# Kernel tuning notes

Hardware: AMD Instinct MI355X
Metric: run time of the kernel (lower is better)

## Reference

```python
import jax, jax.numpy as jnp
import numpy as np

N_ITERATION = 3
NEG_INF = -1e18
EPS = 1e-8


def squash(t, eps=EPS):
    # t: [..., E]; scale = |t|^2/(1+|t|^2), out = scale * t / |t|
    sq = jnp.sum(t * t, axis=-1, keepdims=True)
    return (sq / (1.0 + sq)) * t / (jnp.sqrt(sq) + eps)


def setup_inputs() -> dict:
    key = jax.random.key(0)
    k1, k2, k3, k4 = jax.random.split(key, 4)
    B, K, L, D, O, E = 8, 1024, 1024, 1024, 6, 128
    inputs_u = jax.random.normal(k1, (B, K, D), dtype=jnp.float32)
    context_sequence = jax.random.normal(k2, (B, L, D), dtype=jnp.float32)
    # route_weights: [num_out_caps, d_model, d_per_capsule], fan-in scaled
    route_weights = jax.random.normal(k3, (O, D, E), dtype=jnp.float32) / np.sqrt(D)
    # True = padded in-capsule (masked)
    inputs_mask = jax.random.randint(k4, (B, K), 0, 2).astype(bool)
    return {
        "inputs_u": inputs_u,
        "context_sequence": context_sequence,
        "route_weights": route_weights,
        "inputs_mask": inputs_mask,
    }


def reference(inputs_u, context_sequence, route_weights, inputs_mask):
    # priors_u_hat: [B, K, O, E] (shared route weights across in-capsules)
    priors = jnp.einsum("bkd,ode->bkoe", inputs_u, route_weights)
    B, K, O, E = priors.shape
    L = context_sequence.shape[1]
    logits = jnp.zeros((B, L, K, O), dtype=priors.dtype)
    mask4 = inputs_mask[:, None, :, None]  # [B,1,K,1] -> broadcast to [B,L,K,O]
    outputs_v = None
    probs_c = None
    for i in range(N_ITERATION):
        lg = jnp.where(mask4, NEG_INF, logits)
        probs_c = jax.nn.softmax(lg, axis=-1)  # softmax over out-capsules
        # weighted aggregation over in-capsules then squash: [B,L,O,E]
        outputs_v = squash(jnp.einsum("blko,bkoe->bloe", probs_c, priors))
        if i != N_ITERATION - 1:
            # agreement delta logits: [B,L,K,O]
            logits = logits + jnp.einsum("bkoe,bloe->blko", priors, outputs_v)
    return outputs_v, probs_c
```

## Files before the change

kernel.cpp:

```cpp
#include <hip/hip_runtime.h>
#include <hip/hip_bf16.h>
#include <stdint.h>

typedef __bf16 bf16_t;
typedef __bf16 bf16x8 __attribute__((ext_vector_type(8)));
typedef float f32x4 __attribute__((ext_vector_type(4)));

#define BB 8
#define KK 1024
#define LL 1024
#define DD 1024
#define OO 6
#define EE 128
#define NN 768

__device__ __forceinline__ void async_copy16(const void* gptr, void* lds) {
    __builtin_amdgcn_global_load_lds(
        (__attribute__((address_space(1))) void*)gptr,
        (__attribute__((address_space(3))) void*)lds,
        16, 0, 0);
}

__device__ __forceinline__ void split_bf16(float x, bf16_t& hi, bf16_t& lo) {
    hi = (bf16_t)x;
    lo = (bf16_t)(x - (float)hi);
}

__global__ __launch_bounds__(256) void convert_a(
    const float* __restrict__ A, bf16_t* __restrict__ Ah, bf16_t* __restrict__ Al)
{
    const long i = ((long)blockIdx.x * 256 + threadIdx.x) * 4;
    const float4 x = *(const float4*)(A + i);
    union { bf16_t h[4]; uint2 u; } ph, pl;
    split_bf16(x.x, ph.h[0], pl.h[0]);
    split_bf16(x.y, ph.h[1], pl.h[1]);
    split_bf16(x.z, ph.h[2], pl.h[2]);
    split_bf16(x.w, ph.h[3], pl.h[3]);
    *(uint2*)(Ah + i) = ph.u;
    *(uint2*)(Al + i) = pl.u;
}

__global__ __launch_bounds__(256) void convert_w(
    const float* __restrict__ W, bf16_t* __restrict__ Wth, bf16_t* __restrict__ Wtl)
{
    __shared__ float t[32][33];
    const int o  = blockIdx.z;
    const int d0 = blockIdx.x * 32;
    const int e0 = blockIdx.y * 32;
    const int tx = threadIdx.x & 31;
    const int ty = threadIdx.x >> 5;
    const float* Wo = W + (long)o * DD * EE;
    bf16_t* Ho = Wth + (long)o * EE * DD;
    bf16_t* Lo = Wtl + (long)o * EE * DD;
#pragma unroll
    for (int p = 0; p < 4; ++p)
        t[p * 8 + ty][tx] = Wo[(long)(d0 + p * 8 + ty) * EE + e0 + tx];
    __syncthreads();
#pragma unroll
    for (int p = 0; p < 4; ++p) {
        const float val = t[tx][p * 8 + ty];
        bf16_t h, l;
        split_bf16(val, h, l);
        const long idx = (long)(e0 + p * 8 + ty) * DD + d0 + tx;
        Ho[idx] = h;
        Lo[idx] = l;
    }
}

__global__ __launch_bounds__(256) void gemm_priors(
    const bf16_t* __restrict__ Ah, const bf16_t* __restrict__ Al,
    const bf16_t* __restrict__ Bh, const bf16_t* __restrict__ Bl,
    float* __restrict__ C)
{
    __shared__ alignas(16) bf16_t sAh[128 * 32];
    __shared__ alignas(16) bf16_t sAl[128 * 32];
    __shared__ alignas(16) bf16_t sBh[64 * 32];
    __shared__ alignas(16) bf16_t sBl[64 * 32];

    const int tid  = threadIdx.x;
    const int w    = tid >> 6;
    const int lane = tid & 63;
    const int bm   = blockIdx.x;
    const int bn   = blockIdx.y;
    const int qr   = (w >> 1) * 64;
    const int qc   = (w & 1) * 32;
    const int r16  = lane & 15;
    const int q    = lane >> 4;

    f32x4 acc[4][2] = {};

    const int mrowA = w * 32 + (lane >> 2);
    const int mrowB = w * 16 + (lane >> 2);
    const int kcol  = (lane & 3) * 8;

    const long aoff = (long)(bm * 128 + mrowA) * DD + kcol;
    const long boff = (long)(bn * 64  + mrowB) * DD + kcol;
    const bf16_t* gAh0 = Ah + aoff;  const bf16_t* gAh1 = gAh0 + 16 * DD;
    const bf16_t* gAl0 = Al + aoff;  const bf16_t* gAl1 = gAl0 + 16 * DD;
    const bf16_t* gBh  = Bh + boff;
    const bf16_t* gBl  = Bl + boff;

    bf16_t* lAh0 = sAh + (w * 2 + 0) * 512;
    bf16_t* lAh1 = sAh + (w * 2 + 1) * 512;
    bf16_t* lAl0 = sAl + (w * 2 + 0) * 512;
    bf16_t* lAl1 = sAl + (w * 2 + 1) * 512;
    bf16_t* lBh  = sBh + w * 512;
    bf16_t* lBl  = sBl + w * 512;

    for (int kt = 0; kt < DD / 32; ++kt) {
        const int k0 = kt * 32;
        async_copy16(gAh0 + k0, lAh0);
        async_copy16(gAh1 + k0, lAh1);
        async_copy16(gAl0 + k0, lAl0);
        async_copy16(gAl1 + k0, lAl1);
        async_copy16(gBh  + k0, lBh);
        async_copy16(gBl  + k0, lBl);
        __syncthreads();

        bf16x8 ah[4], al[4], bh[2], bl[2];
#pragma unroll
        for (int i = 0; i < 4; ++i) {
            const int ra = (qr + 16 * i + r16) * 32 + q * 8;
            ah[i] = *(const bf16x8*)(sAh + ra);
            al[i] = *(const bf16x8*)(sAl + ra);
        }
#pragma unroll
        for (int j = 0; j < 2; ++j) {
            const int rb = (qc + 16 * j + r16) * 32 + q * 8;
            bh[j] = *(const bf16x8*)(sBh + rb);
            bl[j] = *(const bf16x8*)(sBl + rb);
        }
#pragma unroll
        for (int i = 0; i < 4; ++i)
#pragma unroll
            for (int j = 0; j < 2; ++j) {
                acc[i][j] = __builtin_amdgcn_mfma_f32_16x16x32_bf16(
                    al[i], bh[j], acc[i][j], 0, 0, 0);
                acc[i][j] = __builtin_amdgcn_mfma_f32_16x16x32_bf16(
                    ah[i], bl[j], acc[i][j], 0, 0, 0);
                acc[i][j] = __builtin_amdgcn_mfma_f32_16x16x32_bf16(
                    ah[i], bh[j], acc[i][j], 0, 0, 0);
            }
        __syncthreads();
    }

#pragma unroll
    for (int i = 0; i < 4; ++i)
#pragma unroll
        for (int j = 0; j < 2; ++j) {
            const int col = bn * 64 + qc + 16 * j + r16;
#pragma unroll
            for (int r = 0; r < 4; ++r) {
                const int row = bm * 128 + qr + 16 * i + q * 4 + r;
                C[(long)row * NN + col] = acc[i][j][r];
            }
        }
}

__global__ __launch_bounds__(256) void s_kernel(
    const float* __restrict__ priors, const float* __restrict__ probs,
    float* __restrict__ s_part, int uniform)
{
    const int bo = blockIdx.x;
    const int b = bo / OO, o = bo % OO;
    const int kbase = blockIdx.y * 128;
    const int t = threadIdx.x;
    const int e = t & 127;
    const int kh = t >> 7;
    float accv = 0.f;
    const int k0 = kbase + kh * 64;
    for (int kk = 0; kk < 64; ++kk) {
        const long row = (long)(b * KK + k0 + kk) * OO + o;
        const float wgt = uniform ? (1.0f / 6.0f) : probs[row];
        accv = fmaf(wgt, priors[row * EE + e], accv);
    }
    __shared__ float red[256];
    red[t] = accv;
    __syncthreads();
    if (t < 128)
        s_part[((long)blockIdx.y * 48 + bo) * EE + e] = red[t] + red[t + 128];
}

__global__ __launch_bounds__(128) void squash_kernel(
    const float* __restrict__ s_part, float* __restrict__ v)
{
    const int bo = blockIdx.x;
    const int e = threadIdx.x;
    float x = 0.f;
#pragma unroll
    for (int y = 0; y < 8; ++y) x += s_part[((long)y * 48 + bo) * EE + e];
    float sq = x * x;
#pragma unroll
    for (int off = 32; off > 0; off >>= 1) sq += __shfl_down(sq, off, 64);
    __shared__ float wsum[2];
    if ((threadIdx.x & 63) == 0) wsum[threadIdx.x >> 6] = sq;
    __syncthreads();
    const float total = wsum[0] + wsum[1];
    v[bo * EE + e] = total / (1.0f + total) * x / (sqrtf(total) + 1e-8f);
}

__global__ __launch_bounds__(256) void fused_pg_kernel(
    const float* __restrict__ priors, const float* __restrict__ v,
    const int* __restrict__ mask, float* __restrict__ g,
    float* __restrict__ probs, int read_g, int store_g)
{
    const int wid  = blockIdx.x * 4 + (threadIdx.x >> 6);
    const int lane = threadIdx.x & 63;
    const int b = wid >> 10;
    const float* pr = priors + (long)wid * NN;
    const float* vb = v + b * NN;

    float po[OO];
#pragma unroll
    for (int o = 0; o < OO; ++o) {
        const int j0 = o * EE + lane;
        po[o] = pr[j0] * vb[j0] + pr[j0 + 64] * vb[j0 + 64];
    }
#pragma unroll
    for (int off = 32; off > 0; off >>= 1)
#pragma unroll
        for (int o = 0; o < OO; ++o) po[o] += __shfl_xor(po[o], off, 64);

    if (read_g) {
#pragma unroll
        for (int o = 0; o < OO; ++o) po[o] += g[wid * OO + o];
    }
    if (store_g && lane < OO) g[wid * OO + lane] = po[lane];

    float p;
    if (mask[wid] != 0) {
        p = 1.0f / 6.0f;
    } else {
        float m = po[0];
#pragma unroll
        for (int o = 1; o < OO; ++o) m = fmaxf(m, po[o]);
        float ssum = 0.f;
#pragma unroll
        for (int o = 0; o < OO; ++o) { po[o] = expf(po[o] - m); ssum += po[o]; }
        const float inv = 1.0f / ssum;
        p = ((lane < OO) ? po[lane] : 0.f) * inv;
    }
    if (lane < OO) probs[wid * OO + lane] = p;
}

__global__ __launch_bounds__(256) void bcast_kernel(
    const float* __restrict__ V, const float* __restrict__ P,
    float* __restrict__ out)
{
    const long base = ((long)blockIdx.x * 256 + threadIdx.x) * 4;
    const long NV = (long)BB * LL * OO * EE;
    const float* src;
    if (base < NV) {
        const long b  = base / ((long)LL * OO * EE);
        const int off = (int)(base % NN);
        src = V + b * NN + off;
    } else {
        const long b2 = base - NV;
        const long b  = b2 / ((long)LL * KK * OO);
        const int off = (int)(b2 % (KK * OO));
        src = P + b * (KK * OO) + off;
    }
    *(float4*)(out + base) = *(const float4*)(src);
}

extern "C" void kernel_launch(void* const* d_in, const int* in_sizes, int n_in,
                              void* d_out, int out_size, void* d_ws, size_t ws_size,
                              hipStream_t stream)
{
    (void)in_sizes; (void)n_in; (void)out_size; (void)ws_size;
    const float* u    = (const float*)d_in[0];
    const float* W    = (const float*)d_in[2];
    const int*   mask = (const int*)d_in[3];
    float*       out  = (float*)d_out;

    char* ws = (char*)d_ws;
    size_t off = 0;
    float*  priors = (float*)(ws + off);  off += (size_t)8192 * NN * 4;
    bf16_t* Ah     = (bf16_t*)(ws + off); off += (size_t)8192 * DD * 2;
    bf16_t* Al     = (bf16_t*)(ws + off); off += (size_t)8192 * DD * 2;
    bf16_t* Wth    = (bf16_t*)(ws + off); off += (size_t)OO * EE * DD * 2;
    bf16_t* Wtl    = (bf16_t*)(ws + off); off += (size_t)OO * EE * DD * 2;
    float*  g      = (float*)(ws + off);  off += (size_t)BB * KK * OO * 4;
    float*  probs  = (float*)(ws + off);  off += (size_t)BB * KK * OO * 4;
    float*  s_part = (float*)(ws + off);  off += (size_t)8 * 48 * EE * 4;
    float*  v      = (float*)(ws + off);

    hipLaunchKernelGGL(convert_a, dim3(8192), dim3(256), 0, stream, u, Ah, Al);
    hipLaunchKernelGGL(convert_w, dim3(32, 4, 6), dim3(256), 0, stream, W, Wth, Wtl);
    hipLaunchKernelGGL(gemm_priors, dim3(64, 12), dim3(256), 0, stream,
                       Ah, Al, Wth, Wtl, priors);

    hipLaunchKernelGGL(s_kernel, dim3(48, 8), dim3(256), 0, stream,
                       priors, (const float*)nullptr, s_part, 1);
    hipLaunchKernelGGL(squash_kernel, dim3(48), dim3(128), 0, stream, s_part, v);

    hipLaunchKernelGGL(fused_pg_kernel, dim3(2048), dim3(256), 0, stream,
                       priors, v, mask, g, probs, 0, 1);
    hipLaunchKernelGGL(s_kernel, dim3(48, 8), dim3(256), 0, stream,
                       priors, probs, s_part, 0);
    hipLaunchKernelGGL(squash_kernel, dim3(48), dim3(128), 0, stream, s_part, v);

    hipLaunchKernelGGL(fused_pg_kernel, dim3(2048), dim3(256), 0, stream,
                       priors, v, mask, g, probs, 1, 0);
    hipLaunchKernelGGL(s_kernel, dim3(48, 8), dim3(256), 0, stream,
                       priors, probs, s_part, 0);
    hipLaunchKernelGGL(squash_kernel, dim3(48), dim3(128), 0, stream, s_part, v);

    hipLaunchKernelGGL(bcast_kernel, dim3(55296), dim3(256), 0, stream, v, probs, out);
}
```

Baseline: 372.7 us.

## Fuse routing iterations into GEMM epilogue and single-pass prob/aggregate kernels

Measured after the change: 376.2 us. No clear change (+1.0%).

```diff
diff --git a/kernel.cpp b/kernel.cpp
--- a/kernel.cpp
+++ b/kernel.cpp
@@ -24,6 +24,18 @@
 __device__ __forceinline__ void split_bf16(float x, bf16_t& hi, bf16_t& lo) {
     hi = (bf16_t)x;
     lo = (bf16_t)(x - (float)hi);
+}
+
+__device__ __forceinline__ void squash_regs(const float* sp, float* vv, int lane) {
+#pragma unroll
+    for (int o = 0; o < 6; ++o) {
+        float t = sp[2*o]*sp[2*o] + sp[2*o+1]*sp[2*o+1];
+#pragma unroll
+        for (int off = 32; off > 0; off >>= 1) t += __shfl_xor(t, off, 64);
+        const float sc = t / (1.0f + t) / (sqrtf(t) + 1e-8f);
+        vv[2*o]   = sc * sp[2*o];
+        vv[2*o+1] = sc * sp[2*o+1];
+    }
 }
 
 __global__ __launch_bounds__(256) void convert_a(
@@ -70,12 +82,13 @@
 __global__ __launch_bounds__(256) void gemm_priors(
     const bf16_t* __restrict__ Ah, const bf16_t* __restrict__ Al,
     const bf16_t* __restrict__ Bh, const bf16_t* __restrict__ Bl,
-    float* __restrict__ C)
+    float* __restrict__ C, float* __restrict__ s0)
 {
     __shared__ alignas(16) bf16_t sAh[128 * 32];
     __shared__ alignas(16) bf16_t sAl[128 * 32];
     __shared__ alignas(16) bf16_t sBh[64 * 32];
     __shared__ alignas(16) bf16_t sBl[64 * 32];
+    __shared__ float sRed[64];
 
     const int tid  = threadIdx.x;
     const int w    = tid >> 6;
@@ -155,112 +168,160 @@
                 C[(long)row * NN + col] = acc[i][j][r];
             }
         }
-}
-
-__global__ __launch_bounds__(256) void s_kernel(
-    const float* __restrict__ priors, const float* __restrict__ probs,
-    float* __restrict__ s_part, int uniform)
-{
-    const int bo = blockIdx.x;
-    const int b = bo / OO, o = bo % OO;
-    const int kbase = blockIdx.y * 128;
+
+    if (tid < 64) sRed[tid] = 0.f;
+    __syncthreads();
+#pragma unroll
+    for (int j = 0; j < 2; ++j) {
+        float cs = 0.f;
+#pragma unroll
+        for (int i = 0; i < 4; ++i)
+            cs += acc[i][j][0] + acc[i][j][1] + acc[i][j][2] + acc[i][j][3];
+        cs += __shfl_xor(cs, 16, 64);
+        cs += __shfl_xor(cs, 32, 64);
+        if (lane < 16)
+            atomicAdd(&sRed[qc + 16 * j + r16], cs);
+    }
+    __syncthreads();
+    if (tid < 64)
+        atomicAdd(&s0[(bm >> 3) * NN + bn * 64 + tid], sRed[tid] * (1.0f / 6.0f));
+}
+
+__global__ __launch_bounds__(256) void pgs_kernel(
+    const float* __restrict__ priors, const float* __restrict__ s_prev,
+    const int* __restrict__ mask, float* __restrict__ g,
+    float* __restrict__ probs, float* __restrict__ s_cur, int first)
+{
+    const int blk  = blockIdx.x;
+    const int b    = blk >> 7;
+    const int k8   = (blk & 127) * 8;
+    const int w    = threadIdx.x >> 6;
+    const int lane = threadIdx.x & 63;
+
+    float vv[12];
+    {
+        float sp[12];
+#pragma unroll
+        for (int s = 0; s < 12; ++s) sp[s] = s_prev[b * NN + s * 64 + lane];
+        squash_regs(sp, vv, lane);
+    }
+
+    float sacc[12];
+#pragma unroll
+    for (int s = 0; s < 12; ++s) sacc[s] = 0.f;
+
+#pragma unroll
+    for (int r = 0; r < 2; ++r) {
+        const int k = k8 + w * 2 + r;
+        const long rid = (long)b * KK + k;
+        const float* pr = priors + rid * NN;
+        float pp[12];
+#pragma unroll
+        for (int s = 0; s < 12; ++s) pp[s] = pr[s * 64 + lane];
+
+        float d[6];
+#pragma unroll
+        for (int o = 0; o < 6; ++o) {
+            float t = pp[2*o] * vv[2*o] + pp[2*o+1] * vv[2*o+1];
+#pragma unroll
+            for (int off = 32; off > 0; off >>= 1) t += __shfl_xor(t, off, 64);
+            d[o] = t;
+        }
+
+        if (first) {
+            if (lane < 6) {
+                float x = d[0];
+#pragma unroll
+                for (int o = 1; o < 6; ++o) if (lane == o) x = d[o];
+                g[rid * 6 + lane] = x;
+            }
+        } else {
+#pragma unroll
+            for (int o = 0; o < 6; ++o) d[o] += g[rid * 6 + o];
+        }
+
+        float p[6];
+        if (mask[rid] != 0) {
+#pragma unroll
+            for (int o = 0; o < 6; ++o) p[o] = 1.0f / 6.0f;
+        } else {
+            float m = d[0];
+#pragma unroll
+            for (int o = 1; o < 6; ++o) m = fmaxf(m, d[o]);
+            float ssum = 0.f;
+#pragma unroll
+            for (int o = 0; o < 6; ++o) { p[o] = expf(d[o] - m); ssum += p[o]; }
+            const float inv = 1.0f / ssum;
+#pragma unroll
+            for (int o = 0; o < 6; ++o) p[o] *= inv;
+        }
+
+        if (!first && lane < 6) {
+            float x = p[0];
+#pragma unroll
+            for (int o = 1; o < 6; ++o) if (lane == o) x = p[o];
+            probs[rid * 6 + lane] = x;
+        }
+
+#pragma unroll
+        for (int s = 0; s < 12; ++s) sacc[s] = fmaf(p[s >> 1], pp[s], sacc[s]);
+    }
+
+    __shared__ float red[4][768];
+#pragma unroll
+    for (int s = 0; s < 12; ++s) red[w][s * 64 + lane] = sacc[s];
+    __syncthreads();
     const int t = threadIdx.x;
-    const int e = t & 127;
-    const int kh = t >> 7;
-    float accv = 0.f;
-    const int k0 = kbase + kh * 64;
-    for (int kk = 0; kk < 64; ++kk) {
-        const long row = (long)(b * KK + k0 + kk) * OO + o;
-        const float wgt = uniform ? (1.0f / 6.0f) : probs[row];
-        accv = fmaf(wgt, priors[row * EE + e], accv);
-    }
-    __shared__ float red[256];
-    red[t] = accv;
-    __syncthreads();
-    if (t < 128)
-        s_part[((long)blockIdx.y * 48 + bo) * EE + e] = red[t] + red[t + 128];
-}
-
-__global__ __launch_bounds__(128) void squash_kernel(
-    const float* __restrict__ s_part, float* __restrict__ v)
-{
-    const int bo = blockIdx.x;
-    const int e = threadIdx.x;
-    float x = 0.f;
-#pragma unroll
-    for (int y = 0; y < 8; ++y) x += s_part[((long)y * 48 + bo) * EE + e];
-    float sq = x * x;
-#pragma unroll
-    for (int off = 32; off > 0; off >>= 1) sq += __shfl_down(sq, off, 64);
-    __shared__ float wsum[2];
-    if ((threadIdx.x & 63) == 0) wsum[threadIdx.x >> 6] = sq;
-    __syncthreads();
-    const float total = wsum[0] + wsum[1];
-    v[bo * EE + e] = total / (1.0f + total) * x / (sqrtf(total) + 1e-8f);
-}
-
-__global__ __launch_bounds__(256) void fused_pg_kernel(
-    const float* __restrict__ priors, const float* __restrict__ v,
-    const int* __restrict__ mask, float* __restrict__ g,
-    float* __restrict__ probs, int read_g, int store_g)
-{
-    const int wid  = blockIdx.x * 4 + (threadIdx.x >> 6);
-    const int lane = threadIdx.x & 63;
-    const int b = wid >> 10;
-    const float* pr = priors + (long)wid * NN;
-    const float* vb = v + b * NN;
-
-    float po[OO];
-#pragma unroll
-    for (int o = 0; o < OO; ++o) {
-        const int j0 = o * EE + lane;
-        po[o] = pr[j0] * vb[j0] + pr[j0 + 64] * vb[j0 + 64];
-    }
-#pragma unroll
-    for (int off = 32; off > 0; off >>= 1)
-#pragma unroll
-        for (int o = 0; o < OO; ++o) po[o] += __shfl_xor(po[o], off, 64);
-
-    if (read_g) {
-#pragma unroll
-        for (int o = 0; o < OO; ++o) po[o] += g[wid * OO + o];
-    }
-    if (store_g && lane < OO) g[wid * OO + lane] = po[lane];
-
-    float p;
-    if (mask[wid] != 0) {
-        p = 1.0f / 6.0f;
+#pragma unroll
+    for (int i = 0; i < 3; ++i) {
+        const int flat = t + i * 256;
+        atomicAdd(&s_cur[b * NN + flat],
+                  red[0][flat] + red[1][flat] + red[2][flat] + red[3][flat]);
+    }
+}
+
+__global__ __launch_bounds__(256) void bcast_kernel(
+    const float* __restrict__ s2, const float* __restrict__ P,
+    float* __restrict__ out)
+{
+    const int blk = blockIdx.x;
+    if (blk < 2048) {
+        const int b  = blk >> 8;
+        const int l0 = (blk & 255) * 4;
+        const int w = threadIdx.x >> 6, lane = threadIdx.x & 63;
+        __shared__ float vrow[768];
+        if (w == 0) {
+            float sp[12], vv[12];
+#pragma unroll
+            for (int s = 0; s < 12; ++s) sp[s] = s2[b * NN + s * 64 + lane];
+            squash_regs(sp, vv, lane);
+#pragma unroll
+            for (int s = 0; s < 12; ++s) vrow[s * 64 + lane] = vv[s];
+        }
+        __syncthreads();
+        float* dst = out + ((long)b * LL + l0) * NN;
+        const int t = threadIdx.x;
+#pragma unroll
+        for (int i = 0; i < 3; ++i) {
+            const int idx = t * 12 + i * 4;
+            *(float4*)(dst + idx) = *(const float4*)(vrow + (idx % NN));
+        }
     } else {
-        float m = po[0];
-#pragma unroll
-        for (int o = 1; o < OO; ++o) m = fmaxf(m, po[o]);
-        float ssum = 0.f;
-#pragma unroll
-        for (int o = 0; o < OO; ++o) { po[o] = expf(po[o] - m); ssum += po[o]; }
-        const float inv = 1.0f / ssum;
-        p = ((lane < OO) ? po[lane] : 0.f) * inv;
-    }
-    if (lane < OO) probs[wid * OO + lane] = p;
-}
-
-__global__ __launch_bounds__(256) void bcast_kernel(
-    const float* __restrict__ V, const float* __restrict__ P,
-    float* __restrict__ out)
-{
-    const long base = ((long)blockIdx.x * 256 + threadIdx.x) * 4;
-    const long NV = (long)BB * LL * OO * EE;
-    const float* src;
-    if (base < NV) {
-        const long b  = base / ((long)LL * OO * EE);
-        const int off = (int)(base % NN);
-        src = V + b * NN + off;
-    } else {
-        const long b2 = base - NV;
-        const long b  = b2 / ((long)LL * KK * OO);
-        const int off = (int)(b2 % (KK * OO));
-        src = P + b * (KK * OO) + off;
-    }
-    *(float4*)(out + base) = *(const float4*)(src);
+        const long NVF = (long)BB * LL * OO * EE;
+        const int blk2 = blk - 2048;
+        const long base = (long)blk2 * 4096;
+        const int b = (int)(base / ((long)LL * KK * OO));
+        const int choff = (int)(base % (KK * OO));
+        const float* src = P + (long)b * (KK * OO);
+        float* dst = out + NVF + base;
+        const int t = threadIdx.x;
+#pragma unroll
+        for (int i = 0; i < 4; ++i) {
+            int off = choff + t * 16 + i * 4;
+            if (off >= KK * OO) off -= KK * OO;
+            *(float4*)(dst + t * 16 + i * 4) = *(const float4*)(src + off);
+        }
+    }
 }
 
 extern "C" void kernel_launch(void* const* d_in, const int* in_sizes, int n_in,
@@ -282,29 +343,18 @@
     bf16_t* Wtl    = (bf16_t*)(ws + off); off += (size_t)OO * EE * DD * 2;
     float*  g      = (float*)(ws + off);  off += (size_t)BB * KK * OO * 4;
     float*  probs  = (float*)(ws + off);  off += (size_t)BB * KK * OO * 4;
-    float*  s_part = (float*)(ws + off);  off += (size_t)8 * 48 * EE * 4;
-    float*  v      = (float*)(ws + off);
-
+    float*  sbuf   = (float*)(ws + off);  off += (size_t)3 * BB * NN * 4;
+    float*  s0 = sbuf, *s1 = sbuf + BB * NN, *s2 = sbuf + 2 * BB * NN;
+
+    hipMemsetAsync(sbuf, 0, 3 * BB * NN * sizeof(float), stream);
     hipLaunchKernelGGL(convert_a, dim3(8192), dim3(256), 0, stream, u, Ah, Al);
     hipLaunchKernelGGL(convert_w, dim3(32, 4, 6), dim3(256), 0, stream, W, Wth, Wtl);
     hipLaunchKernelGGL(gemm_priors, dim3(64, 12), dim3(256), 0, stream,
-                       Ah, Al, Wth, Wtl, priors);
-
-    hipLaunchKernelGGL(s_kernel, dim3(48, 8), dim3(256), 0, stream,
-                       priors, (const float*)nullptr, s_part, 1);
-    hipLaunchKernelGGL(squash_kernel, dim3(48), dim3(128), 0, stream, s_part, v);
-
-    hipLaunchKernelGGL(fused_pg_kernel, dim3(2048), dim3(256), 0, stream,
-                       priors, v, mask, g, probs, 0, 1);
-    hipLaunchKernelGGL(s_kernel, dim3(48, 8), dim3(256), 0, stream,
-                       priors, probs, s_part, 0);
-    hipLaunchKernelGGL(squash_kernel, dim3(48), dim3(128), 0, stream, s_part, v);
-
-    hipLaunchKernelGGL(fused_pg_kernel, dim3(2048), dim3(256), 0, stream,
-                       priors, v, mask, g, probs, 1, 0);
-    hipLaunchKernelGGL(s_kernel, dim3(48, 8), dim3(256), 0, stream,
-                       priors, probs, s_part, 0);
-    hipLaunchKernelGGL(squash_kernel, dim3(48), dim3(128), 0, stream, s_part, v);
-
-    hipLaunchKernelGGL(bcast_kernel, dim3(55296), dim3(256), 0, stream, v, probs, out);
-}
+                       Ah, Al, Wth, Wtl, priors, s0);
+    hipLaunchKernelGGL(pgs_kernel, dim3(1024), dim3(256), 0, stream,
+                       priors, s0, mask, g, probs, s1, 1);
+    hipLaunchKernelGGL(pgs_kernel, dim3(1024), dim3(256), 0, stream,
+                       priors, s1, mask, g, probs, s2, 0);
+    hipLaunchKernelGGL(bcast_kernel, dim3(14336), dim3(256), 0, stream,
+                       s2, probs, out);
+}
```
